# Kernel optimization log

Hardware: AMD Instinct MI355X
Metric: run time of the kernel (lower is better)

## Reference

```python
import jax, jax.numpy as jnp
import numpy as np

IMG = 1024.0
MAXD = 8.0
EPS = 1e-6
ENC_HEADS = 12
DEC_HEADS = 16


def _ln(x, w, b):
    m = jnp.mean(x, -1, keepdims=True)
    v = jnp.mean((x - m) ** 2, -1, keepdims=True)
    return (x - m) / jnp.sqrt(v + EPS) * w + b


def _attn(x, qkv_w, qkv_b, pr_w, pr_b, nh, key_mask):
    B, L, D = x.shape
    hd = D // nh
    qkv = (x @ qkv_w + qkv_b).reshape(B, L, 3, nh, hd).transpose(2, 0, 3, 1, 4)
    q, k, v = qkv[0], qkv[1], qkv[2]  # [B, nh, L, hd]
    s = jnp.einsum('bhqd,bhkd->bhqk', q, k) * (hd ** -0.5)
    if key_mask is not None:
        # restrict attention to visible tokens; identical math to per-sample gather+encode
        s = jnp.where(key_mask[:, None, None, :], s, -1e9)
    a = jax.nn.softmax(s, -1)
    o = jnp.einsum('bhqk,bhkd->bhqd', a, v).transpose(0, 2, 1, 3).reshape(B, L, D)
    return o @ pr_w + pr_b


def _block(x, i, ln1w, ln1b, qkvw, qkvb, prw, prb, ln2w, ln2b, f1w, f1b, f2w, f2b, nh, key_mask):
    x = x + _attn(_ln(x, ln1w[i], ln1b[i]), qkvw[i], qkvb[i], prw[i], prb[i], nh, key_mask)
    h = jax.nn.gelu(_ln(x, ln2w[i], ln2b[i]) @ f1w[i] + f1b[i], approximate=False)
    return x + h @ f2w[i] + f2b[i]


def _pos(coords, depths, w1, b1, w2, b2):
    x1, x2, y1, y2 = coords[..., 0], coords[..., 1], coords[..., 2], coords[..., 3]
    f = jnp.stack([(x1 + x2) / 2.0 / IMG, (y1 + y2) / 2.0 / IMG,
                   (x2 - x1) / IMG, (y2 - y1) / IMG, depths / MAXD], -1)
    return jax.nn.gelu(f @ w1 + b1, approximate=False) @ w2 + b2


def _forward(patches, coords, depths, pe_w, pe_b, pos1_w, pos1_b, pos2_w, pos2_b,
             e_ln1_w, e_ln1_b, e_qkv_w, e_qkv_b, e_pr_w, e_pr_b, e_ln2_w, e_ln2_b,
             e_f1_w, e_f1_b, e_f2_w, e_f2_b, enorm_w, enorm_b,
             de_w, de_b, mask_token, dpos1_w, dpos1_b, dpos2_w, dpos2_b,
             d_ln1_w, d_ln1_b, d_qkv_w, d_qkv_b, d_pr_w, d_pr_b, d_ln2_w, d_ln2_b,
             d_f1_w, d_f1_b, d_f2_w, d_f2_b, dnorm_w, dnorm_b,
             hi_w, hi_b, hn_w, hn_b, mask):
    B, L = mask.shape
    x = patches.reshape(B, L, -1) @ pe_w + pe_b + _pos(coords, depths, pos1_w, pos1_b, pos2_w, pos2_b)
    visible = (mask == 0)
    h = x
    for i in range(e_qkv_w.shape[0]):
        h = _block(h, i, e_ln1_w, e_ln1_b, e_qkv_w, e_qkv_b, e_pr_w, e_pr_b,
                   e_ln2_w, e_ln2_b, e_f1_w, e_f1_b, e_f2_w, e_f2_b, ENC_HEADS, visible)
    encoded = jnp.where(visible[..., None], _ln(h, enorm_w, enorm_b), 0.0)
    xd = encoded @ de_w + de_b
    xd = jnp.where((mask != 0)[..., None], mask_token, xd)
    xd = xd + _pos(coords, depths, dpos1_w, dpos1_b, dpos2_w, dpos2_b)
    for i in range(d_qkv_w.shape[0]):
        xd = _block(xd, i, d_ln1_w, d_ln1_b, d_qkv_w, d_qkv_b, d_pr_w, d_pr_b,
                    d_ln2_w, d_ln2_b, d_f1_w, d_f1_b, d_f2_w, d_f2_b, DEC_HEADS, None)
    xd = _ln(xd, dnorm_w, dnorm_b)
    return (xd @ hi_w + hi_b, xd @ hn_w + hn_b)


def setup_inputs() -> dict:
    key = jax.random.key(0)
    ks = iter(jax.random.split(key, 80))
    def nrm(shape, std=0.02):
        return jax.random.normal(next(ks), shape, jnp.float32) * std
    B, L, P, C = 4, 512, 32, 1
    D, DD = 768, 512
    ED, DDEP = 12, 8
    pd = C * P * P
    inp = {}
    inp['patches'] = jax.random.normal(next(ks), (B, L, C, P, P), jnp.float32)
    inp['coords'] = jax.random.uniform(next(ks), (B, L, 4), jnp.float32)
    inp['depths'] = jax.random.uniform(next(ks), (B, L), jnp.float32)
    inp['mask'] = jax.random.randint(next(ks), (B, L), 0, 2, jnp.int32)
    inp['pe_w'] = nrm((pd, D)); inp['pe_b'] = jnp.zeros((D,))
    inp['pos1_w'] = nrm((5, D // 2)); inp['pos1_b'] = jnp.zeros((D // 2,))
    inp['pos2_w'] = nrm((D // 2, D)); inp['pos2_b'] = jnp.zeros((D,))
    inp['e_ln1_w'] = jnp.ones((ED, D)); inp['e_ln1_b'] = jnp.zeros((ED, D))
    inp['e_qkv_w'] = nrm((ED, D, 3 * D)); inp['e_qkv_b'] = jnp.zeros((ED, 3 * D))
    inp['e_pr_w'] = nrm((ED, D, D)); inp['e_pr_b'] = jnp.zeros((ED, D))
    inp['e_ln2_w'] = jnp.ones((ED, D)); inp['e_ln2_b'] = jnp.zeros((ED, D))
    inp['e_f1_w'] = nrm((ED, D, 4 * D)); inp['e_f1_b'] = jnp.zeros((ED, 4 * D))
    inp['e_f2_w'] = nrm((ED, 4 * D, D)); inp['e_f2_b'] = jnp.zeros((ED, D))
    inp['enorm_w'] = jnp.ones((D,)); inp['enorm_b'] = jnp.zeros((D,))
    inp['de_w'] = nrm((D, DD)); inp['de_b'] = jnp.zeros((DD,))
    inp['mask_token'] = nrm((DD,))
    inp['dpos1_w'] = nrm((5, DD // 2)); inp['dpos1_b'] = jnp.zeros((DD // 2,))
    inp['dpos2_w'] = nrm((DD // 2, DD)); inp['dpos2_b'] = jnp.zeros((DD,))
    inp['d_ln1_w'] = jnp.ones((DDEP, DD)); inp['d_ln1_b'] = jnp.zeros((DDEP, DD))
    inp['d_qkv_w'] = nrm((DDEP, DD, 3 * DD)); inp['d_qkv_b'] = jnp.zeros((DDEP, 3 * DD))
    inp['d_pr_w'] = nrm((DDEP, DD, DD)); inp['d_pr_b'] = jnp.zeros((DDEP, DD))
    inp['d_ln2_w'] = jnp.ones((DDEP, DD)); inp['d_ln2_b'] = jnp.zeros((DDEP, DD))
    inp['d_f1_w'] = nrm((DDEP, DD, 4 * DD)); inp['d_f1_b'] = jnp.zeros((DDEP, 4 * DD))
    inp['d_f2_w'] = nrm((DDEP, 4 * DD, DD)); inp['d_f2_b'] = jnp.zeros((DDEP, DD))
    inp['dnorm_w'] = jnp.ones((DD,)); inp['dnorm_b'] = jnp.zeros((DD,))
    inp['hi_w'] = nrm((DD, pd)); inp['hi_b'] = jnp.zeros((pd,))
    inp['hn_w'] = nrm((DD, pd)); inp['hn_b'] = jnp.zeros((pd,))
    return inp


def reference(patches, coords, depths, pe_w, pe_b, pos1_w, pos1_b, pos2_w, pos2_b,
              e_ln1_w, e_ln1_b, e_qkv_w, e_qkv_b, e_pr_w, e_pr_b, e_ln2_w, e_ln2_b,
              e_f1_w, e_f1_b, e_f2_w, e_f2_b, enorm_w, enorm_b,
              de_w, de_b, mask_token, dpos1_w, dpos1_b, dpos2_w, dpos2_b,
              d_ln1_w, d_ln1_b, d_qkv_w, d_qkv_b, d_pr_w, d_pr_b, d_ln2_w, d_ln2_b,
              d_f1_w, d_f1_b, d_f2_w, d_f2_b, dnorm_w, dnorm_b,
              hi_w, hi_b, hn_w, hn_b, mask):
    return _forward(patches, coords, depths, pe_w, pe_b, pos1_w, pos1_b, pos2_w, pos2_b,
                    e_ln1_w, e_ln1_b, e_qkv_w, e_qkv_b, e_pr_w, e_pr_b, e_ln2_w, e_ln2_b,
                    e_f1_w, e_f1_b, e_f2_w, e_f2_b, enorm_w, enorm_b,
                    de_w, de_b, mask_token, dpos1_w, dpos1_b, dpos2_w, dpos2_b,
                    d_ln1_w, d_ln1_b, d_qkv_w, d_qkv_b, d_pr_w, d_pr_b, d_ln2_w, d_ln2_b,
                    d_f1_w, d_f1_b, d_f2_w, d_f2_b, dnorm_w, dnorm_b,
                    hi_w, hi_b, hn_w, hn_b, mask)
```

## Files before the change

kernel.cpp:

```cpp
#include <hip/hip_runtime.h>
#include <hip/hip_bf16.h>

using bf16 = __hip_bfloat16;
typedef __bf16 bf16x8 __attribute__((ext_vector_type(8)));
typedef float f32x4 __attribute__((ext_vector_type(4)));

__device__ __forceinline__ float gelu_exact(float x) {
    return 0.5f * x * (1.0f + erff(x * 0.70710678118654752440f));
}

#define GLD_LDS16(g, l) __builtin_amdgcn_global_load_lds( \
    (__attribute__((address_space(1))) void*)(g),          \
    (__attribute__((address_space(3))) void*)(l), 16, 0, 0)

#define WAITV(n) asm volatile("s_waitcnt vmcnt(" #n ")" ::: "memory")

template<int BM,int BN,int WM,int WN,int FM,int FN,int OUT_BF16,int HAS_BIAS,int HAS_RES,int DO_GELU>
__global__ __launch_bounds__(256, 4) void gemm_bt(
    const bf16* __restrict__ A, long lda,
    const bf16* __restrict__ Bt, long ldb,
    void* __restrict__ Cv, long ldc,
    const float* __restrict__ bias, const float* __restrict__ Res,
    int K, float alpha)
{
    static_assert(WM * WN == 4 && BM == WM * FM * 16 && BN == WN * FN * 16, "cfg");
    __shared__ alignas(16) unsigned short As[4][BM * 32];
    __shared__ alignas(16) unsigned short Bs[4][BN * 32];

    const int nwg = gridDim.x * gridDim.y;
    const int orig = blockIdx.y * gridDim.x + blockIdx.x;
    const int q = nwg >> 3, r = nwg & 7;
    const int xcd = orig & 7, seq = orig >> 3;
    const int wg = (xcd < r ? xcd * (q + 1) : r * (q + 1) + (xcd - r) * q) + seq;
    const int bn0 = (wg % gridDim.x) * BN;
    const int bm0 = (wg / gridDim.x) * BM;

    const int tid = threadIdx.x;
    const int wave = tid >> 6, lane = tid & 63;
    const int wm = (wave / WN) * (FM * 16);
    const int wn = (wave % WN) * (FN * 16);

    f32x4 acc[FM][FN] = {};

    constexpr int CA = BM / 16, CT = (BM + BN) / 16;
    constexpr int LPT = CT / 4;
    static_assert(CT % 4 == 0 && (LPT == 2 || LPT == 3), "stage cfg");
    const int lrow = lane >> 2;
    const int lcol = (((lane & 3) ^ ((lrow >> 1) & 3)) * 8);
    const int nk = K >> 5;

    const int fr = lane & 15;
    const int kg = lane >> 4;
    const int kswz = (kg ^ ((fr >> 1) & 3)) * 8;

    auto stage = [&](int buf, int kt) {
        const int k0 = kt * 32;
        for (int c = wave; c < CT; c += 4) {
            if (c < CA) {
                const bf16* src = A + (long)(bm0 + c * 16 + lrow) * lda + k0 + lcol;
                GLD_LDS16(src, &As[buf][c * 512]);
            } else {
                const int c2 = c - CA;
                const bf16* src = Bt + (long)(bn0 + c2 * 16 + lrow) * ldb + k0 + lcol;
                GLD_LDS16(src, &Bs[buf][c2 * 512]);
            }
        }
    };

    for (int i = 0; i < 4 && i < nk; ++i) stage(i, i);

    for (int kt = 0; kt < nk; ++kt) {
        const int cur = kt & 3;
        int r3 = nk - 1 - kt; if (r3 > 3) r3 = 3;
        if constexpr (LPT == 2) {
            switch (r3) { case 3: WAITV(6); break; case 2: WAITV(4); break;
                          case 1: WAITV(2); break; default: WAITV(0); }
        } else {
            switch (r3) { case 3: WAITV(9); break; case 2: WAITV(6); break;
                          case 1: WAITV(3); break; default: WAITV(0); }
        }
        __builtin_amdgcn_s_barrier();
        __builtin_amdgcn_sched_barrier(0);

        bf16x8 af[FM], bfv[FN];
        #pragma unroll
        for (int m = 0; m < FM; ++m)
            af[m] = *(const bf16x8*)&As[cur][(wm + m * 16 + fr) * 32 + kswz];
        #pragma unroll
        for (int n = 0; n < FN; ++n)
            bfv[n] = *(const bf16x8*)&Bs[cur][(wn + n * 16 + fr) * 32 + kswz];
        #pragma unroll
        for (int m = 0; m < FM; ++m)
            #pragma unroll
            for (int n = 0; n < FN; ++n)
                acc[m][n] = __builtin_amdgcn_mfma_f32_16x16x32_bf16(af[m], bfv[n], acc[m][n], 0, 0, 0);

        __builtin_amdgcn_sched_barrier(0);
        asm volatile("s_waitcnt lgkmcnt(0)" ::: "memory");
        __builtin_amdgcn_s_barrier();
        if (kt + 4 < nk) stage(cur, kt + 4);
    }

    const int r0 = (lane >> 4) * 4;
    #pragma unroll
    for (int m = 0; m < FM; ++m) {
        const int rowb = bm0 + wm + m * 16 + r0;
        #pragma unroll
        for (int n = 0; n < FN; ++n) {
            const int col = bn0 + wn + n * 16 + fr;
            #pragma unroll
            for (int j = 0; j < 4; ++j) {
                float v = acc[m][n][j] * alpha;
                if (HAS_BIAS) v += bias[col];
                if (HAS_RES)  v += Res[(long)(rowb + j) * ldc + col];
                if (DO_GELU)  v = gelu_exact(v);
                const long idx = (long)(rowb + j) * ldc + col;
                if (OUT_BF16) ((bf16*)Cv)[idx] = __float2bfloat16(v);
                else          ((float*)Cv)[idx] = v;
            }
        }
    }
}

#define GEMM_A(OB,HB,HR,DG) gemm_bt<64,128,2,2,2,4, OB,HB,HR,DG>
#define GEMM_B(OB,HB,HR,DG) gemm_bt<64,64,2,2,2,2, OB,HB,HR,DG>

template<int HD, int MASKED>
__global__ __launch_bounds__(256) void flash_attn(
    const bf16* __restrict__ qkv, int ldq, int Doff, int nh,
    const bf16* __restrict__ Vt,
    bf16* __restrict__ Out, int ldo,
    const int* __restrict__ mask, float alpha)
{
    constexpr int KVT = 256, KS = HD + 8, SV = KVT + 8;
    __shared__ unsigned short Ks[KVT * KS];
    __shared__ unsigned short Vs[HD * SV];
    __shared__ unsigned short Pl[4][16 * 40];

    const int bh = blockIdx.y, b = bh / nh, h = bh % nh;
    const int tid = threadIdx.x;
    const int wave = tid >> 6, lane = tid & 63;
    const int q0 = blockIdx.x * 64 + wave * 16;
    const int fr = lane & 15, kg = lane >> 4;

    const bf16* Qb = qkv + ((long)(b * 512 + q0 + fr)) * ldq + h * HD;
    bf16x8 af[HD / 32];
    #pragma unroll
    for (int kc = 0; kc < HD / 32; ++kc)
        af[kc] = *(const bf16x8*)(Qb + kc * 32 + kg * 8);

    const bf16* Kg = qkv + (long)b * 512 * ldq + Doff + h * HD;
    const bf16* Vg = Vt + (long)bh * HD * 512;
    const int* mg = mask + (long)b * 512;

    float m[4], l[4];
    f32x4 O[HD / 16] = {};
    #pragma unroll
    for (int j = 0; j < 4; ++j) { m[j] = -INFINITY; l[j] = 0.f; }

    for (int t = 0; t < 512; t += KVT) {
        __syncthreads();
        for (int i = tid; i < KVT * (HD / 8); i += 256) {
            const int rr = i / (HD / 8), c = i % (HD / 8);
            *(bf16x8*)&Ks[rr * KS + c * 8] = *(const bf16x8*)(Kg + (long)(t + rr) * ldq + c * 8);
        }
        for (int i = tid; i < HD * (KVT / 8); i += 256) {
            const int d = i / (KVT / 8), c = i % (KVT / 8);
            *(bf16x8*)&Vs[d * SV + c * 8] = *(const bf16x8*)(Vg + (long)d * 512 + t + c * 8);
        }
        __syncthreads();

        for (int n0 = 0; n0 < KVT; n0 += 32) {
            f32x4 s[2];
            int msk[2] = {0, 0};
            #pragma unroll
            for (int f = 0; f < 2; ++f) {
                f32x4 a = {};
                #pragma unroll
                for (int kc = 0; kc < HD / 32; ++kc) {
                    bf16x8 kb = *(const bf16x8*)&Ks[(n0 + f * 16 + fr) * KS + kc * 32 + kg * 8];
                    a = __builtin_amdgcn_mfma_f32_16x16x32_bf16(af[kc], kb, a, 0, 0, 0);
                }
                #pragma unroll
                for (int j = 0; j < 4; ++j) a[j] *= alpha;
                s[f] = a;
                if (MASKED) msk[f] = mg[t + n0 + f * 16 + fr];
            }
            float g[4], p0[4], p1[4];
            #pragma unroll
            for (int j = 0; j < 4; ++j) {
                float t4 = fmaxf(s[0][j], s[1][j]);
                t4 = fmaxf(t4, __shfl_xor(t4, 1));
                t4 = fmaxf(t4, __shfl_xor(t4, 2));
                t4 = fmaxf(t4, __shfl_xor(t4, 4));
                t4 = fmaxf(t4, __shfl_xor(t4, 8));
                const float mn = fmaxf(m[j], t4);
                g[j] = __expf(m[j] - mn);
                p0[j] = msk[0] ? 0.f : __expf(s[0][j] - mn);
                p1[j] = msk[1] ? 0.f : __expf(s[1][j] - mn);
                float rs = p0[j] + p1[j];
                rs += __shfl_xor(rs, 1);
                rs += __shfl_xor(rs, 2);
                rs += __shfl_xor(rs, 4);
                rs += __shfl_xor(rs, 8);
                l[j] = l[j] * g[j] + rs;
                m[j] = mn;
            }
            #pragma unroll
            for (int dt = 0; dt < HD / 16; ++dt)
                #pragma unroll
                for (int j = 0; j < 4; ++j) O[dt][j] *= g[j];
            unsigned short* pl = &Pl[wave][0];
            #pragma unroll
            for (int j = 0; j < 4; ++j) {
                bf16 b0 = __float2bfloat16(p0[j]);
                bf16 b1 = __float2bfloat16(p1[j]);
                pl[(kg * 4 + j) * 40 + fr]      = *(unsigned short*)&b0;
                pl[(kg * 4 + j) * 40 + 16 + fr] = *(unsigned short*)&b1;
            }
            __builtin_amdgcn_sched_barrier(0);
            bf16x8 pa = *(const bf16x8*)&pl[fr * 40 + kg * 8];
            #pragma unroll
            for (int dt = 0; dt < HD / 16; ++dt) {
                bf16x8 vb = *(const bf16x8*)&Vs[(dt * 16 + fr) * SV + n0 + kg * 8];
                O[dt] = __builtin_amdgcn_mfma_f32_16x16x32_bf16(pa, vb, O[dt], 0, 0, 0);
            }
        }
    }

    float inv[4];
    #pragma unroll
    for (int j = 0; j < 4; ++j) inv[j] = 1.0f / l[j];
    #pragma unroll
    for (int dt = 0; dt < HD / 16; ++dt)
        #pragma unroll
        for (int j = 0; j < 4; ++j) {
            const long row = (long)b * 512 + q0 + kg * 4 + j;
            Out[row * ldo + h * HD + dt * 16 + fr] = __float2bfloat16(O[dt][j] * inv[j]);
        }
}

__global__ void transpose_cast_b(const float* __restrict__ in, bf16* __restrict__ out,
                                 int K, int N, int Kpad, long inS, long outS)
{
    __shared__ float tile[32][33];
    in  += (long)blockIdx.z * inS;
    out += (long)blockIdx.z * outS;
    const int n0 = blockIdx.x * 32, k0 = blockIdx.y * 32;
    const int tx = threadIdx.x & 31, ty = threadIdx.x >> 5;
    #pragma unroll
    for (int r = 0; r < 4; ++r) {
        const int k = k0 + ty + r * 8, n = n0 + tx;
        tile[ty + r * 8][tx] = (k < K && n < N) ? in[(long)k * N + n] : 0.0f;
    }
    __syncthreads();
    #pragma unroll
    for (int r = 0; r < 4; ++r) {
        const int n = n0 + ty + r * 8, k = k0 + tx;
        if (n < N && k < Kpad)
            out[(long)n * Kpad + k] = __float2bfloat16(tile[tx][ty + r * 8]);
    }
}

template<int Dd, int MASKED>
__global__ __launch_bounds__(256) void ln_wave(
    const float* __restrict__ X, const float* __restrict__ w, const float* __restrict__ b,
    bf16* __restrict__ Y, const int* __restrict__ mask)
{
    const int wave = threadIdx.x >> 6, lane = threadIdx.x & 63;
    const int t = blockIdx.x * 4 + wave;
    const float* x = X + (long)t * Dd;
    constexpr int NE = Dd / 64;
    float v[NE];
    float s = 0.f, s2 = 0.f;
    #pragma unroll
    for (int k = 0; k < NE; ++k) {
        v[k] = x[lane + k * 64];
        s += v[k]; s2 += v[k] * v[k];
    }
    #pragma unroll
    for (int o = 32; o; o >>= 1) { s += __shfl_xor(s, o); s2 += __shfl_xor(s2, o); }
    const float mean = s / Dd;
    const float var = s2 / Dd - mean * mean;
    const float inv = 1.0f / sqrtf(var + 1e-6f);
    const bool zero = MASKED && (mask[t] != 0);
    #pragma unroll
    for (int k = 0; k < NE; ++k) {
        const int c = lane + k * 64;
        const float rr = zero ? 0.0f : ((v[k] - mean) * inv * w[c] + b[c]);
        Y[(long)t * Dd + c] = __float2bfloat16(rr);
    }
}

__global__ void repack_v(const unsigned short* __restrict__ qkv, int ldq, int Doff, int nh, int hd,
                         unsigned short* __restrict__ Vt)
{
    __shared__ unsigned short tile[32][33];
    const int bh = blockIdx.z, b = bh / nh, h = bh % nh;
    const int l0 = blockIdx.x * 32, d0 = blockIdx.y * 32;
    const int tx = threadIdx.x & 31, ty = threadIdx.x >> 5;
    const unsigned short* src = qkv + (long)b * 512 * ldq + 2 * Doff + h * hd;
    #pragma unroll
    for (int r = 0; r < 4; ++r)
        tile[ty + r * 8][tx] = src[(long)(l0 + ty + r * 8) * ldq + d0 + tx];
    __syncthreads();
    unsigned short* dst = Vt + (long)bh * hd * 512;
    #pragma unroll
    for (int r = 0; r < 4; ++r)
        dst[(long)(d0 + ty + r * 8) * 512 + l0 + tx] = tile[tx][ty + r * 8];
}

__global__ void build_feat(const float* __restrict__ coords, const float* __restrict__ depths,
                           bf16* __restrict__ F)
{
    const int t = blockIdx.x * 256 + threadIdx.x;
    if (t >= 2048) return;
    const float* c = coords + t * 4;
    float f[5];
    f[0] = (c[0] + c[1]) * 0.5f / 1024.0f;
    f[1] = (c[2] + c[3]) * 0.5f / 1024.0f;
    f[2] = (c[1] - c[0]) / 1024.0f;
    f[3] = (c[3] - c[2]) / 1024.0f;
    f[4] = depths[t] / 8.0f;
    bf16* o = F + (long)t * 32;
    #pragma unroll
    for (int j = 0; j < 32; ++j)
        o[j] = __float2bfloat16(j < 5 ? f[j] : 0.0f);
}

__global__ void conv_patches(const float* __restrict__ in, bf16* __restrict__ out, int n)
{
    const int i = blockIdx.x * 256 + threadIdx.x;
    if (i < n) out[i] = __float2bfloat16(in[i]);
}

__global__ void mask_pos_add(float* __restrict__ xd, const float* __restrict__ posD,
                             const int* __restrict__ mask, const float* __restrict__ token)
{
    const int i = blockIdx.x * 256 + threadIdx.x;
    const int t = i >> 9, c = i & 511;
    const float v = (mask[t] != 0) ? token[c] : xd[i];
    xd[i] = v + posD[i];
}

extern "C" void kernel_launch(void* const* d_in, const int* in_sizes, int n_in,
                              void* d_out, int out_size, void* d_ws, size_t ws_size,
                              hipStream_t stream)
{
    (void)in_sizes; (void)n_in; (void)out_size;
    const int D = 768, DD = 512;

    const float* patches    = (const float*)d_in[0];
    const float* coords     = (const float*)d_in[1];
    const float* depths     = (const float*)d_in[2];
    const int*   mask       = (const int*)d_in[3];
    const float* pe_w       = (const float*)d_in[4];
    const float* pe_b       = (const float*)d_in[5];
    const float* pos1_w     = (const float*)d_in[6];
    const float* pos1_b     = (const float*)d_in[7];
    const float* pos2_w     = (const float*)d_in[8];
    const float* pos2_b     = (const float*)d_in[9];
    const float* e_ln1_w    = (const float*)d_in[10];
    const float* e_ln1_b    = (const float*)d_in[11];
    const float* e_qkv_w    = (const float*)d_in[12];
    const float* e_qkv_b    = (const float*)d_in[13];
    const float* e_pr_w     = (const float*)d_in[14];
    const float* e_pr_b     = (const float*)d_in[15];
    const float* e_ln2_w    = (const float*)d_in[16];
    const float* e_ln2_b    = (const float*)d_in[17];
    const float* e_f1_w     = (const float*)d_in[18];
    const float* e_f1_b     = (const float*)d_in[19];
    const float* e_f2_w     = (const float*)d_in[20];
    const float* e_f2_b     = (const float*)d_in[21];
    const float* enorm_w    = (const float*)d_in[22];
    const float* enorm_b    = (const float*)d_in[23];
    const float* de_w       = (const float*)d_in[24];
    const float* de_b       = (const float*)d_in[25];
    const float* mask_token = (const float*)d_in[26];
    const float* dpos1_w    = (const float*)d_in[27];
    const float* dpos1_b    = (const float*)d_in[28];
    const float* dpos2_w    = (const float*)d_in[29];
    const float* dpos2_b    = (const float*)d_in[30];
    const float* d_ln1_w    = (const float*)d_in[31];
    const float* d_ln1_b    = (const float*)d_in[32];
    const float* d_qkv_w    = (const float*)d_in[33];
    const float* d_qkv_b    = (const float*)d_in[34];
    const float* d_pr_w     = (const float*)d_in[35];
    const float* d_pr_b     = (const float*)d_in[36];
    const float* d_ln2_w    = (const float*)d_in[37];
    const float* d_ln2_b    = (const float*)d_in[38];
    const float* d_f1_w     = (const float*)d_in[39];
    const float* d_f1_b     = (const float*)d_in[40];
    const float* d_f2_w     = (const float*)d_in[41];
    const float* d_f2_b     = (const float*)d_in[42];
    const float* dnorm_w    = (const float*)d_in[43];
    const float* dnorm_b    = (const float*)d_in[44];
    const float* hi_w       = (const float*)d_in[45];
    const float* hi_b       = (const float*)d_in[46];
    const float* hn_w       = (const float*)d_in[47];
    const float* hn_b       = (const float*)d_in[48];

    char* p = (char*)d_ws;
    auto alloc = [&](size_t bytes) -> char* {
        char* r = p; p += (bytes + 255) & ~(size_t)255; return r;
    };
    bf16* pe_wt  = (bf16*)alloc(768L * 1024 * 2);
    bf16* pos1t  = (bf16*)alloc(384L * 32 * 2);
    bf16* pos2t  = (bf16*)alloc(768L * 384 * 2);
    bf16* dpos1t = (bf16*)alloc(256L * 32 * 2);
    bf16* dpos2t = (bf16*)alloc(512L * 256 * 2);
    bf16* de_t   = (bf16*)alloc(512L * 768 * 2);
    bf16* hi_t   = (bf16*)alloc(1024L * 512 * 2);
    bf16* hn_t   = (bf16*)alloc(1024L * 512 * 2);
    bf16* wslot  = (bf16*)alloc(3072L * 768 * 2);
    bf16*  feat    = (bf16*)alloc(2048L * 32 * 2);
    bf16*  patchbf = (bf16*)alloc(2048L * 1024 * 2);
    bf16*  poshE   = (bf16*)alloc(2048L * 384 * 2);
    float* posE    = (float*)alloc(2048L * 768 * 4);
    bf16*  poshD   = (bf16*)alloc(2048L * 256 * 2);
    float* posD    = (float*)alloc(2048L * 512 * 4);
    float* xbuf    = (float*)alloc(2048L * 768 * 4);
    bf16*  lnbuf   = (bf16*)alloc(2048L * 768 * 2);
    bf16*  qkvbuf  = (bf16*)alloc(2048L * 2304 * 2);
    bf16*  hid     = (bf16*)alloc(2048L * 3072 * 2);
    bf16*  Vt      = (bf16*)alloc(48L * 64 * 512 * 2);
    bf16*  pin     = (bf16*)alloc(2048L * 768 * 2);
    float* xd      = (float*)alloc(2048L * 512 * 4);

    const size_t bigBytes =
        (12L*2304*768 + 12L*768*768 + 12L*3072*768 + 12L*768*3072 +
          8L*1536*512 +  8L*512*512 +  8L*2048*512 +  8L*512*2048) * 2 + 8 * 256;
    const size_t used = (size_t)(p - (char*)d_ws);
    const bool batched = ws_size >= used + bigBytes;
    bf16 *eqkvt = nullptr, *eprt = nullptr, *ef1t = nullptr, *ef2t = nullptr;
    bf16 *dqkvt = nullptr, *dprt = nullptr, *df1t = nullptr, *df2t = nullptr;
    if (batched) {
        eqkvt = (bf16*)alloc(12L * 2304 * 768 * 2);
        eprt  = (bf16*)alloc(12L * 768 * 768 * 2);
        ef1t  = (bf16*)alloc(12L * 3072 * 768 * 2);
        ef2t  = (bf16*)alloc(12L * 768 * 3072 * 2);
        dqkvt = (bf16*)alloc(8L * 1536 * 512 * 2);
        dprt  = (bf16*)alloc(8L * 512 * 512 * 2);
        df1t  = (bf16*)alloc(8L * 2048 * 512 * 2);
        df2t  = (bf16*)alloc(8L * 512 * 2048 * 2);
    }

    conv_patches<<<8192, 256, 0, stream>>>(patches, patchbf, 2097152);
    build_feat<<<8, 256, 0, stream>>>(coords, depths, feat);

    auto trb = [&](const float* in, bf16* out, int K, int N, int Kpad, int z) {
        dim3 g((N + 31) / 32, (Kpad + 31) / 32, z);
        transpose_cast_b<<<g, 256, 0, stream>>>(in, out, K, N, Kpad, (long)K * N, (long)N * Kpad);
    };
    trb(pe_w,    pe_wt,  1024,  768, 1024, 1);
    trb(pos1_w,  pos1t,     5,  384,   32, 1);
    trb(pos2_w,  pos2t,   384,  768,  384, 1);
    trb(dpos1_w, dpos1t,    5,  256,   32, 1);
    trb(dpos2_w, dpos2t,  256,  512,  256, 1);
    trb(de_w,    de_t,    768,  512,  768, 1);
    trb(hi_w,    hi_t,    512, 1024,  512, 1);
    trb(hn_w,    hn_t,    512, 1024,  512, 1);
    if (batched) {
        trb(e_qkv_w, eqkvt, 768, 2304, 768, 12);
        trb(e_pr_w,  eprt,  768,  768, 768, 12);
        trb(e_f1_w,  ef1t,  768, 3072, 768, 12);
        trb(e_f2_w,  ef2t, 3072,  768, 3072, 12);
        trb(d_qkv_w, dqkvt, 512, 1536, 512, 8);
        trb(d_pr_w,  dprt,  512,  512, 512, 8);
        trb(d_f1_w,  df1t,  512, 2048, 512, 8);
        trb(d_f2_w,  df2t, 2048,  512, 2048, 8);
    }
    auto wsl = [&](const float* src, long off, int K, int N, int Kpad) -> const bf16* {
        dim3 g((N + 31) / 32, (Kpad + 31) / 32, 1);
        transpose_cast_b<<<g, 256, 0, stream>>>(src + off, wslot, K, N, Kpad, 0, 0);
        return wslot;
    };

    GEMM_B(1,1,0,1)<<<dim3(6,32,1),256,0,stream>>>(
        feat, 32, pos1t, 32, poshE, 384, pos1_b, nullptr, 32, 1.0f);
    GEMM_B(0,1,0,0)<<<dim3(12,32,1),256,0,stream>>>(
        poshE, 384, pos2t, 384, posE, 768, pos2_b, nullptr, 384, 1.0f);
    GEMM_B(1,1,0,1)<<<dim3(4,32,1),256,0,stream>>>(
        feat, 32, dpos1t, 32, poshD, 256, dpos1_b, nullptr, 32, 1.0f);
    GEMM_B(0,1,0,0)<<<dim3(8,32,1),256,0,stream>>>(
        poshD, 256, dpos2t, 256, posD, 512, dpos2_b, nullptr, 256, 1.0f);

    GEMM_B(0,1,1,0)<<<dim3(12,32,1),256,0,stream>>>(
        patchbf, 1024, pe_wt, 1024, xbuf, 768, pe_b, posE, 1024, 1.0f);

    for (int i = 0; i < 12; ++i) {
        ln_wave<768,0><<<512,256,0,stream>>>(xbuf, e_ln1_w + i*D, e_ln1_b + i*D, lnbuf, nullptr);
        const bf16* Wq = batched ? eqkvt + (long)i*2304*768
                                 : wsl(e_qkv_w, (long)i*768*2304, 768, 2304, 768);
        GEMM_A(1,1,0,0)<<<dim3(18,32,1),256,0,stream>>>(
            lnbuf, 768, Wq, 768, qkvbuf, 2304, e_qkv_b + i*2304, nullptr, 768, 1.0f);
        repack_v<<<dim3(16,2,48),256,0,stream>>>(
            (const unsigned short*)qkvbuf, 2304, 768, 12, 64, (unsigned short*)Vt);
        flash_attn<64,1><<<dim3(8,48),256,0,stream>>>(
            qkvbuf, 2304, 768, 12, Vt, pin, 768, mask, 0.125f);
        const bf16* Wp = batched ? eprt + (long)i*768*768
                                 : wsl(e_pr_w, (long)i*768*768, 768, 768, 768);
        GEMM_B(0,1,1,0)<<<dim3(12,32,1),256,0,stream>>>(
            pin, 768, Wp, 768, xbuf, 768, e_pr_b + i*768, xbuf, 768, 1.0f);
        ln_wave<768,0><<<512,256,0,stream>>>(xbuf, e_ln2_w + i*D, e_ln2_b + i*D, lnbuf, nullptr);
        const bf16* W1 = batched ? ef1t + (long)i*3072*768
                                 : wsl(e_f1_w, (long)i*768*3072, 768, 3072, 768);
        GEMM_A(1,1,0,1)<<<dim3(24,32,1),256,0,stream>>>(
            lnbuf, 768, W1, 768, hid, 3072, e_f1_b + i*3072, nullptr, 768, 1.0f);
        const bf16* W2 = batched ? ef2t + (long)i*768*3072
                                 : wsl(e_f2_w, (long)i*3072*768, 3072, 768, 3072);
        GEMM_B(0,1,1,0)<<<dim3(12,32,1),256,0,stream>>>(
            hid, 3072, W2, 3072, xbuf, 768, e_f2_b + i*768, xbuf, 3072, 1.0f);
    }

    ln_wave<768,1><<<512,256,0,stream>>>(xbuf, enorm_w, enorm_b, lnbuf, mask);
    GEMM_B(0,1,0,0)<<<dim3(8,32,1),256,0,stream>>>(
        lnbuf, 768, de_t, 768, xd, 512, de_b, nullptr, 768, 1.0f);
    mask_pos_add<<<4096,256,0,stream>>>(xd, posD, mask, mask_token);

    for (int i = 0; i < 8; ++i) {
        ln_wave<512,0><<<512,256,0,stream>>>(xd, d_ln1_w + i*DD, d_ln1_b + i*DD, lnbuf, nullptr);
        const bf16* Wq = batched ? dqkvt + (long)i*1536*512
                                 : wsl(d_qkv_w, (long)i*512*1536, 512, 1536, 512);
        GEMM_A(1,1,0,0)<<<dim3(12,32,1),256,0,stream>>>(
            lnbuf, 512, Wq, 512, qkvbuf, 1536, d_qkv_b + i*1536, nullptr, 512, 1.0f);
        repack_v<<<dim3(16,1,64),256,0,stream>>>(
            (const unsigned short*)qkvbuf, 1536, 512, 16, 32, (unsigned short*)Vt);
        flash_attn<32,0><<<dim3(8,64),256,0,stream>>>(
            qkvbuf, 1536, 512, 16, Vt, pin, 512, nullptr, 0.17677669529663687f);
        const bf16* Wp = batched ? dprt + (long)i*512*512
                                 : wsl(d_pr_w, (long)i*512*512, 512, 512, 512);
        GEMM_B(0,1,1,0)<<<dim3(8,32,1),256,0,stream>>>(
            pin, 512, Wp, 512, xd, 512, d_pr_b + i*512, xd, 512, 1.0f);
        ln_wave<512,0><<<512,256,0,stream>>>(xd, d_ln2_w + i*DD, d_ln2_b + i*DD, lnbuf, nullptr);
        const bf16* W1 = batched ? df1t + (long)i*2048*512
                                 : wsl(d_f1_w, (long)i*512*2048, 512, 2048, 512);
        GEMM_A(1,1,0,1)<<<dim3(16,32,1),256,0,stream>>>(
            lnbuf, 512, W1, 512, hid, 2048, d_f1_b + i*2048, nullptr, 512, 1.0f);
        const bf16* W2 = batched ? df2t + (long)i*512*2048
                                 : wsl(d_f2_w, (long)i*2048*512, 2048, 512, 2048);
        GEMM_B(0,1,1,0)<<<dim3(8,32,1),256,0,stream>>>(
            hid, 2048, W2, 2048, xd, 512, d_f2_b + i*512, xd, 2048, 1.0f);
    }

    ln_wave<512,0><<<512,256,0,stream>>>(xd, dnorm_w, dnorm_b, lnbuf, nullptr);
    float* outp = (float*)d_out;
    GEMM_B(0,1,0,0)<<<dim3(16,32,1),256,0,stream>>>(
        lnbuf, 512, hi_t, 512, outp, 1024, hi_b, nullptr, 512, 1.0f);
    GEMM_B(0,1,0,0)<<<dim3(16,32,1),256,0,stream>>>(
        lnbuf, 512, hn_t, 512, outp + 2097152, 1024, hn_b, nullptr, 512, 1.0f);
}
```

Baseline: 2.922 ms.

## Fuse V transpose into flash attention and merge output head GEMMs

Removes the separate repack_v kernel and its Vt scratch buffer. Flash attention now reads V rows straight from the QKV buffer and transposes them into shared memory with scalar 2-byte stores, which may cause LDS bank conflicts and a slower staging loop. The two final head projections are merged into one 32-column-block GEMM launch whose epilogue routes columns to the two output halves with the matching bias. That merge assumes the hi_t and hn_t transposed weights sit contiguously in memory.

```diff
diff --git a/kernel.cpp b/kernel.cpp
--- a/kernel.cpp
+++ b/kernel.cpp
@@ -15,7 +15,7 @@
 
 #define WAITV(n) asm volatile("s_waitcnt vmcnt(" #n ")" ::: "memory")
 
-template<int BM,int BN,int WM,int WN,int FM,int FN,int OUT_BF16,int HAS_BIAS,int HAS_RES,int DO_GELU>
+template<int BM,int BN,int WM,int WN,int FM,int FN,int OUT_BF16,int HAS_BIAS,int HAS_RES,int DO_GELU,int HEADS>
 __global__ __launch_bounds__(256, 4) void gemm_bt(
     const bf16* __restrict__ A, long lda,
     const bf16* __restrict__ Bt, long ldb,
@@ -111,6 +111,14 @@
             #pragma unroll
             for (int j = 0; j < 4; ++j) {
                 float v = acc[m][n][j] * alpha;
+                if (HEADS) {
+                    v += (col < 1024) ? bias[col] : ((const float*)Res)[col - 1024];
+                    const long idx = (col < 1024)
+                        ? (long)(rowb + j) * 1024 + col
+                        : 2097152L + (long)(rowb + j) * 1024 + (col - 1024);
+                    ((float*)Cv)[idx] = v;
+                    continue;
+                }
                 if (HAS_BIAS) v += bias[col];
                 if (HAS_RES)  v += Res[(long)(rowb + j) * ldc + col];
                 if (DO_GELU)  v = gelu_exact(v);
@@ -122,13 +130,13 @@
     }
 }
 
-#define GEMM_A(OB,HB,HR,DG) gemm_bt<64,128,2,2,2,4, OB,HB,HR,DG>
-#define GEMM_B(OB,HB,HR,DG) gemm_bt<64,64,2,2,2,2, OB,HB,HR,DG>
+#define GEMM_A(OB,HB,HR,DG) gemm_bt<64,128,2,2,2,4, OB,HB,HR,DG,0>
+#define GEMM_B(OB,HB,HR,DG) gemm_bt<64,64,2,2,2,2, OB,HB,HR,DG,0>
+#define GEMM_H              gemm_bt<64,64,2,2,2,2, 0,1,0,0,1>
 
 template<int HD, int MASKED>
 __global__ __launch_bounds__(256) void flash_attn(
     const bf16* __restrict__ qkv, int ldq, int Doff, int nh,
-    const bf16* __restrict__ Vt,
     bf16* __restrict__ Out, int ldo,
     const int* __restrict__ mask, float alpha)
 {
@@ -150,7 +158,7 @@
         af[kc] = *(const bf16x8*)(Qb + kc * 32 + kg * 8);
 
     const bf16* Kg = qkv + (long)b * 512 * ldq + Doff + h * HD;
-    const bf16* Vg = Vt + (long)bh * HD * 512;
+    const bf16* Vg = qkv + (long)b * 512 * ldq + 2 * Doff + h * HD;
     const int* mg = mask + (long)b * 512;
 
     float m[4], l[4];
@@ -164,9 +172,14 @@
             const int rr = i / (HD / 8), c = i % (HD / 8);
             *(bf16x8*)&Ks[rr * KS + c * 8] = *(const bf16x8*)(Kg + (long)(t + rr) * ldq + c * 8);
         }
-        for (int i = tid; i < HD * (KVT / 8); i += 256) {
-            const int d = i / (KVT / 8), c = i % (KVT / 8);
-            *(bf16x8*)&Vs[d * SV + c * 8] = *(const bf16x8*)(Vg + (long)d * 512 + t + c * 8);
+        for (int i = tid; i < KVT * (HD / 8); i += 256) {
+            const int ll = i / (HD / 8), c = i % (HD / 8);
+            bf16x8 vv = *(const bf16x8*)(Vg + (long)(t + ll) * ldq + c * 8);
+            #pragma unroll
+            for (int j = 0; j < 8; ++j) {
+                bf16 e = ((const bf16*)&vv)[j];
+                Vs[(c * 8 + j) * SV + ll] = *(unsigned short*)&e;
+            }
         }
         __syncthreads();
 
@@ -290,24 +303,6 @@
         const float rr = zero ? 0.0f : ((v[k] - mean) * inv * w[c] + b[c]);
         Y[(long)t * Dd + c] = __float2bfloat16(rr);
     }
-}
-
-__global__ void repack_v(const unsigned short* __restrict__ qkv, int ldq, int Doff, int nh, int hd,
-                         unsigned short* __restrict__ Vt)
-{
-    __shared__ unsigned short tile[32][33];
-    const int bh = blockIdx.z, b = bh / nh, h = bh % nh;
-    const int l0 = blockIdx.x * 32, d0 = blockIdx.y * 32;
-    const int tx = threadIdx.x & 31, ty = threadIdx.x >> 5;
-    const unsigned short* src = qkv + (long)b * 512 * ldq + 2 * Doff + h * hd;
-    #pragma unroll
-    for (int r = 0; r < 4; ++r)
-        tile[ty + r * 8][tx] = src[(long)(l0 + ty + r * 8) * ldq + d0 + tx];
-    __syncthreads();
-    unsigned short* dst = Vt + (long)bh * hd * 512;
-    #pragma unroll
-    for (int r = 0; r < 4; ++r)
-        dst[(long)(d0 + ty + r * 8) * 512 + l0 + tx] = tile[tx][ty + r * 8];
 }
 
 __global__ void build_feat(const float* __restrict__ coords, const float* __restrict__ depths,
@@ -423,7 +418,6 @@
     bf16*  lnbuf   = (bf16*)alloc(2048L * 768 * 2);
     bf16*  qkvbuf  = (bf16*)alloc(2048L * 2304 * 2);
     bf16*  hid     = (bf16*)alloc(2048L * 3072 * 2);
-    bf16*  Vt      = (bf16*)alloc(48L * 64 * 512 * 2);
     bf16*  pin     = (bf16*)alloc(2048L * 768 * 2);
     float* xd      = (float*)alloc(2048L * 512 * 4);
 
@@ -494,10 +488,8 @@
                                  : wsl(e_qkv_w, (long)i*768*2304, 768, 2304, 768);
         GEMM_A(1,1,0,0)<<<dim3(18,32,1),256,0,stream>>>(
             lnbuf, 768, Wq, 768, qkvbuf, 2304, e_qkv_b + i*2304, nullptr, 768, 1.0f);
-        repack_v<<<dim3(16,2,48),256,0,stream>>>(
-            (const unsigned short*)qkvbuf, 2304, 768, 12, 64, (unsigned short*)Vt);
         flash_attn<64,1><<<dim3(8,48),256,0,stream>>>(
-            qkvbuf, 2304, 768, 12, Vt, pin, 768, mask, 0.125f);
+            qkvbuf, 2304, 768, 12, pin, 768, mask, 0.125f);
         const bf16* Wp = batched ? eprt + (long)i*768*768
                                  : wsl(e_pr_w, (long)i*768*768, 768, 768, 768);
         GEMM_B(0,1,1,0)<<<dim3(12,32,1),256,0,stream>>>(
@@ -524,10 +516,8 @@
                                  : wsl(d_qkv_w, (long)i*512*1536, 512, 1536, 512);
         GEMM_A(1,1,0,0)<<<dim3(12,32,1),256,0,stream>>>(
             lnbuf, 512, Wq, 512, qkvbuf, 1536, d_qkv_b + i*1536, nullptr, 512, 1.0f);
-        repack_v<<<dim3(16,1,64),256,0,stream>>>(
-            (const unsigned short*)qkvbuf, 1536, 512, 16, 32, (unsigned short*)Vt);
         flash_attn<32,0><<<dim3(8,64),256,0,stream>>>(
-            qkvbuf, 1536, 512, 16, Vt, pin, 512, nullptr, 0.17677669529663687f);
+            qkvbuf, 1536, 512, 16, pin, 512, nullptr, 0.17677669529663687f);
         const bf16* Wp = batched ? dprt + (long)i*512*512
                                  : wsl(d_pr_w, (long)i*512*512, 512, 512, 512);
         GEMM_B(0,1,1,0)<<<dim3(8,32,1),256,0,stream>>>(
@@ -544,9 +534,6 @@
     }
 
     ln_wave<512,0><<<512,256,0,stream>>>(xd, dnorm_w, dnorm_b, lnbuf, nullptr);
-    float* outp = (float*)d_out;
-    GEMM_B(0,1,0,0)<<<dim3(16,32,1),256,0,stream>>>(
-        lnbuf, 512, hi_t, 512, outp, 1024, hi_b, nullptr, 512, 1.0f);
-    GEMM_B(0,1,0,0)<<<dim3(16,32,1),256,0,stream>>>(
-        lnbuf, 512, hn_t, 512, outp + 2097152, 1024, hn_b, nullptr, 512, 1.0f);
-}
+    GEMM_H<<<dim3(32,32,1),256,0,stream>>>(
+        lnbuf, 512, hi_t, 512, (float*)d_out, 1024, hi_b, (const float*)hn_b, 512, 1.0f);
+}
```

After: 2.900 ms. Within noise of the previous version (-0.8%).
